# Kernel tuning notes

Hardware: AMD Instinct MI355X
Metric: run time of the kernel (lower is better)

## Reference

```python
import jax, jax.numpy as jnp
import numpy as np

H = 2048
NH = 16
DH = H // NH
EPS = 1e-05


def setup_inputs() -> dict:
    key = jax.random.key(0)
    ks = jax.random.split(key, 12)
    B, S, A = 4, 2048, 512
    s = 1.0 / np.sqrt(H)
    inp = {
        "hidden_states": jax.random.normal(ks[0], (B, S, H), jnp.float32),
        "audio_tokens": jax.random.normal(ks[1], (B, A, H), jnp.float32),
        "attention_mask": jax.random.randint(ks[2], (B, A), 0, 2).astype(jnp.float32),
        "Wq": jax.random.normal(ks[3], (H, H), jnp.float32) * s,
        "bq": jnp.zeros((H,), jnp.float32),
        "Wk": jax.random.normal(ks[4], (H, H), jnp.float32) * s,
        "bk": jnp.zeros((H,), jnp.float32),
        "Wv": jax.random.normal(ks[5], (H, H), jnp.float32) * s,
        "bv": jnp.zeros((H,), jnp.float32),
        "Wo": jax.random.normal(ks[6], (H, H), jnp.float32) * s,
        "bo": jnp.zeros((H,), jnp.float32),
        "gamma": jnp.ones((H,), jnp.float32),
        "beta": jnp.zeros((H,), jnp.float32),
    }
    return inp


def reference(hidden_states, audio_tokens, attention_mask,
              Wq, bq, Wk, bk, Wv, bv, Wo, bo, gamma, beta):
    B, S, _ = hidden_states.shape
    A = audio_tokens.shape[1]
    # projections (weights stored [in, out])
    q = (hidden_states @ Wq + bq).reshape(B, S, NH, DH)
    k = (audio_tokens @ Wk + bk).reshape(B, A, NH, DH)
    v = (audio_tokens @ Wv + bv).reshape(B, A, NH, DH)
    # scores: [B, NH, S, A]
    scores = jnp.einsum('bqhd,bkhd->bhqk', q, k) / np.sqrt(DH)
    scores = scores + attention_mask[:, None, None, :] * -10000.0
    probs = jax.nn.softmax(scores, axis=-1)
    # context: [B, S, NH, DH] -> [B, S, H]
    ctx = jnp.einsum('bhqk,bkhd->bqhd', probs, v).reshape(B, S, H)
    out = ctx @ Wo + bo
    # residual + LayerNorm
    x = out + hidden_states
    mu = jnp.mean(x, axis=-1, keepdims=True)
    var = jnp.mean(jnp.square(x - mu), axis=-1, keepdims=True)
    return (x - mu) * jax.lax.rsqrt(var + EPS) * gamma + beta
```

## Files before the change

kernel.cpp:

```cpp
#include <hip/hip_runtime.h>

#define HDIM 2048
#define NHEAD 16
#define DHEAD 128
#define BATCH 4
#define SEQ 2048
#define AUD 512

typedef unsigned short u16;
typedef unsigned int u32;
typedef __bf16 bf16_t;
typedef bf16_t bf16x8 __attribute__((ext_vector_type(8)));
typedef short short8 __attribute__((ext_vector_type(8)));
typedef float f32x4 __attribute__((ext_vector_type(4)));

typedef const __attribute__((address_space(1))) u32 gas_u32;
typedef __attribute__((address_space(3))) u32 las_u32;

__device__ __forceinline__ float b2f(u16 h) {
  union { u32 u; float f; } v; v.u = ((u32)h) << 16; return v.f;
}
__device__ __forceinline__ u16 f2b(float f) {
  union { float f; u32 u; } v; v.f = f;
  u32 r = (v.u + 0x7FFFu + ((v.u >> 16) & 1u)) >> 16;
  return (u16)r;
}

__global__ __launch_bounds__(256) void cvt2_k(const float* __restrict__ s0,
                                              u16* __restrict__ d0, int n0,
                                              const float* __restrict__ s1,
                                              u16* __restrict__ d1, int n1) {
  int i = blockIdx.x * 256 + threadIdx.x;
  const float* src; u16* dst; int j;
  if (i < n0) { src = s0; dst = d0; j = i; }
  else { j = i - n0; if (j >= n1) return; src = s1; dst = d1; }
  const float4* s4 = (const float4*)src;
  float4 a = s4[2 * j], b = s4[2 * j + 1];
  short8 o;
  o[0] = (short)f2b(a.x); o[1] = (short)f2b(a.y);
  o[2] = (short)f2b(a.z); o[3] = (short)f2b(a.w);
  o[4] = (short)f2b(b.x); o[5] = (short)f2b(b.y);
  o[6] = (short)f2b(b.z); o[7] = (short)f2b(b.w);
  *(short8*)(dst + (size_t)j * 8) = o;
}

__global__ __launch_bounds__(256) void transpose4_k(
    const float* __restrict__ Wq, const float* __restrict__ Wk,
    const float* __restrict__ Wv, const float* __restrict__ Wo,
    u16* __restrict__ dst4) {
  const float* src = (blockIdx.z == 0) ? Wq
                   : (blockIdx.z == 1) ? Wk
                   : (blockIdx.z == 2) ? Wv : Wo;
  u16* dst = dst4 + (size_t)blockIdx.z * HDIM * HDIM;
  __shared__ float tile[32][33];
  int tx = threadIdx.x, ty = threadIdx.y;
  int x = blockIdx.x * 32 + tx;
  int y0 = blockIdx.y * 32;
#pragma unroll
  for (int j = 0; j < 32; j += 8)
    tile[ty + j][tx] = src[(size_t)(y0 + ty + j) * HDIM + x];
  __syncthreads();
  int x2 = y0 + tx;
  int y2 = blockIdx.x * 32;
#pragma unroll
  for (int j = 0; j < 32; j += 8)
    dst[(size_t)(y2 + ty + j) * HDIM + x2] = f2b(tile[tx][ty + j]);
}

__global__ __launch_bounds__(256) void gemm_bt(
    const u16* __restrict__ A, int lda,
    const u16* __restrict__ Bt, int ldb,
    void* __restrict__ Cv, int ldc,
    const float* __restrict__ bias, float alpha, int M, int N, int K, int cmode) {
  __shared__ u16 As[128 * 32];
  __shared__ u16 Bs[128 * 32];

  int lane = threadIdx.x & 63;
  int wave = threadIdx.x >> 6;
  int gdx = gridDim.x;
  int id = blockIdx.y * gdx + blockIdx.x;
  int cpx = (gdx * gridDim.y) >> 3;
  int sid = (id & 7) * cpx + (id >> 3);
  int m0 = (sid / gdx) * 128;
  int n0 = (sid % gdx) * 128;
  int wm = (wave & 1) * 64;
  int wn = (wave >> 1) * 64;
  int row16 = lane & 15;
  int quad = lane >> 4;

  int sr = (lane >> 2);
  int sc = (lane & 3) * 8;

  f32x4 acc[4][4];
#pragma unroll
  for (int i = 0; i < 4; i++)
#pragma unroll
    for (int j = 0; j < 4; j++) acc[i][j] = (f32x4){0.f, 0.f, 0.f, 0.f};

  for (int k0 = 0; k0 < K; k0 += 32) {
#pragma unroll
    for (int t = 0; t < 2; t++) {
      int chunk = wave * 2 + t;
      int r = chunk * 16 + sr;
      const u16* ga = A + (size_t)(m0 + r) * lda + k0 + sc;
      const u16* gb = Bt + (size_t)(n0 + r) * ldb + k0 + sc;
      __builtin_amdgcn_global_load_lds((gas_u32*)ga, (las_u32*)(As + chunk * 512), 16, 0, 0);
      __builtin_amdgcn_global_load_lds((gas_u32*)gb, (las_u32*)(Bs + chunk * 512), 16, 0, 0);
    }
    __syncthreads();

    short8 af[4], bf[4];
#pragma unroll
    for (int mt = 0; mt < 4; mt++)
      af[mt] = *(const short8*)(As + (wm + mt * 16 + row16) * 32 + quad * 8);
#pragma unroll
    for (int nt = 0; nt < 4; nt++)
      bf[nt] = *(const short8*)(Bs + (wn + nt * 16 + row16) * 32 + quad * 8);
#pragma unroll
    for (int mt = 0; mt < 4; mt++)
#pragma unroll
      for (int nt = 0; nt < 4; nt++)
        acc[mt][nt] = __builtin_amdgcn_mfma_f32_16x16x32_bf16(
            __builtin_bit_cast(bf16x8, af[mt]), __builtin_bit_cast(bf16x8, bf[nt]),
            acc[mt][nt], 0, 0, 0);
    __syncthreads();
  }

#pragma unroll
  for (int nt = 0; nt < 4; nt++) {
    int nn = n0 + wn + nt * 16 + row16;
    float bv = bias ? bias[nn] : 0.f;
#pragma unroll
    for (int mt = 0; mt < 4; mt++) {
#pragma unroll
      for (int r = 0; r < 4; r++) {
        int mm = m0 + wm + mt * 16 + quad * 4 + r;
        float val = (acc[mt][nt][r] + bv) * alpha;
        if (cmode == 2) {
          ((float*)Cv)[(size_t)mm * ldc + nn] = val;
        } else if (cmode == 1) {
          int bb = mm >> 9, aa = mm & 511;
          int hh = nn >> 7, dd = nn & 127;
          ((u16*)Cv)[((size_t)((bb * 16 + hh) * 128 + dd)) * 512 + aa] = f2b(val);
        } else {
          ((u16*)Cv)[(size_t)mm * ldc + nn] = f2b(val);
        }
      }
    }
  }
}

__global__ __launch_bounds__(512, 2) void gemm_ring8(
    const u16* __restrict__ A, int lda,
    const u16* __restrict__ Bt, int ldb,
    void* __restrict__ Cv, int ldc,
    const float* __restrict__ bias, float alpha, int K, int cmode) {
  __shared__ u16 As[4][256 * 32];
  __shared__ u16 Bs[4][256 * 32];

  int tid = threadIdx.x;
  int lane = tid & 63, wave = tid >> 6;
  int wr = wave >> 2, wc = wave & 3;
  int row16 = lane & 15, quad = lane >> 4;
  int cofs = (quad * 8) ^ (((row16 >> 1) & 3) << 3);

  int gdx = gridDim.x;
  int id = blockIdx.y * gdx + blockIdx.x;
  int cpx = (gdx * gridDim.y) >> 3;
  int sid = (id & 7) * cpx + (id >> 3);
  int n0 = (sid % gdx) * 256;
  int m0 = (sid / gdx) * 256;

  int r0 = tid >> 2;
  int c0 = ((tid & 3) ^ ((r0 >> 1) & 3)) * 8;

  f32x4 acc[8][4];
#pragma unroll
  for (int i = 0; i < 8; i++)
#pragma unroll
    for (int j = 0; j < 4; j++) acc[i][j] = (f32x4){0.f, 0.f, 0.f, 0.f};

  auto stageA = [&](int slot, int k0) {
#pragma unroll
    for (int l = 0; l < 2; l++) {
      int row = l * 128 + r0;
      __builtin_amdgcn_global_load_lds(
          (gas_u32*)(A + (size_t)(m0 + row) * lda + k0 + c0),
          (las_u32*)(&As[slot][(l * 512 + tid) * 8]), 16, 0, 0);
    }
  };
  auto stageB = [&](int slot, int k0) {
#pragma unroll
    for (int l = 0; l < 2; l++) {
      int row = l * 128 + r0;
      __builtin_amdgcn_global_load_lds(
          (gas_u32*)(Bt + (size_t)(n0 + row) * ldb + k0 + c0),
          (las_u32*)(&Bs[slot][(l * 512 + tid) * 8]), 16, 0, 0);
    }
  };

  int NT = K >> 5;
  stageA(0, 0);  stageB(0, 0);
  stageA(1, 32); stageB(1, 32);
  stageA(2, 64); stageB(2, 64);
  asm volatile("s_waitcnt vmcnt(8)" ::: "memory");
  __builtin_amdgcn_s_barrier();

  for (int kt = 0; kt < NT; ++kt) {
    int slot = kt & 3;
    int sp = (kt + 3) & 3;
    bool pf = (kt + 3) < NT;
    const u16* as = &As[slot][0];
    const u16* bs = &Bs[slot][0];

    short8 bfr[4], af[4];
#pragma unroll
    for (int ni = 0; ni < 4; ni++)
      bfr[ni] = *(const short8*)(bs + (wc * 64 + ni * 16 + row16) * 32 + cofs);
#pragma unroll
    for (int mi = 0; mi < 4; mi++)
      af[mi] = *(const short8*)(as + (wr * 128 + mi * 16 + row16) * 32 + cofs);
    if (pf) stageA(sp, (kt + 3) << 5);
    __builtin_amdgcn_s_barrier();
    asm volatile("s_waitcnt lgkmcnt(0)" ::: "memory");
    __builtin_amdgcn_s_setprio(1);
#pragma unroll
    for (int mi = 0; mi < 4; mi++)
#pragma unroll
      for (int ni = 0; ni < 4; ni++)
        acc[mi][ni] = __builtin_amdgcn_mfma_f32_16x16x32_bf16(
            __builtin_bit_cast(bf16x8, af[mi]), __builtin_bit_cast(bf16x8, bfr[ni]),
            acc[mi][ni], 0, 0, 0);
    __builtin_amdgcn_s_setprio(0);
    __builtin_amdgcn_s_barrier();

    short8 ag[4];
#pragma unroll
    for (int mi = 0; mi < 4; mi++)
      ag[mi] = *(const short8*)(as + (wr * 128 + (mi + 4) * 16 + row16) * 32 + cofs);
    if (pf) stageB(sp, (kt + 3) << 5);
    {
      int nf = NT - 2 - kt;
      if (nf >= 2)      asm volatile("s_waitcnt vmcnt(8)" ::: "memory");
      else if (nf == 1) asm volatile("s_waitcnt vmcnt(4)" ::: "memory");
      else              asm volatile("s_waitcnt vmcnt(0)" ::: "memory");
    }
    __builtin_amdgcn_s_barrier();
    asm volatile("s_waitcnt lgkmcnt(0)" ::: "memory");
    __builtin_amdgcn_s_setprio(1);
#pragma unroll
    for (int mi = 0; mi < 4; mi++)
#pragma unroll
      for (int ni = 0; ni < 4; ni++)
        acc[mi + 4][ni] = __builtin_amdgcn_mfma_f32_16x16x32_bf16(
            __builtin_bit_cast(bf16x8, ag[mi]), __builtin_bit_cast(bf16x8, bfr[ni]),
            acc[mi + 4][ni], 0, 0, 0);
    __builtin_amdgcn_s_setprio(0);
    __builtin_amdgcn_s_barrier();
  }

#pragma unroll
  for (int ni = 0; ni < 4; ni++) {
    int nn = n0 + wc * 64 + ni * 16 + row16;
    float bv = bias ? bias[nn] : 0.f;
#pragma unroll
    for (int mi = 0; mi < 8; mi++) {
#pragma unroll
      for (int r = 0; r < 4; r++) {
        int mm = m0 + wr * 128 + mi * 16 + quad * 4 + r;
        float val = (acc[mi][ni][r] + bv) * alpha;
        if (cmode == 2) ((float*)Cv)[(size_t)mm * ldc + nn] = val;
        else            ((u16*)Cv)[(size_t)mm * ldc + nn] = f2b(val);
      }
    }
  }
}

__global__ __launch_bounds__(256) void flash_k(
    const u16* __restrict__ Q, const u16* __restrict__ K,
    const u16* __restrict__ Vt, const float* __restrict__ mask,
    u16* __restrict__ Ctx) {
  __shared__ u16 KP[128 * 128];
  __shared__ u16 Vs[128 * 128];

  int bh = blockIdx.y, b = bh >> 4, h = bh & 15;
  int q0 = blockIdx.x * 128;
  int lane = threadIdx.x & 63, wave = threadIdx.x >> 6;
  int row16 = lane & 15, quad = lane >> 4;
  int wq = wave * 32;
  int swr = (row16 & 7) << 3;

  const u16* qbase = Q + ((size_t)(b * SEQ + q0)) * HDIM + h * DHEAD;
  const u16* kbase = K + ((size_t)b * AUD) * HDIM + h * DHEAD;
  const u16* vbase = Vt + ((size_t)(b * NHEAD + h)) * DHEAD * AUD;
  const float* mp = mask + b * AUD;

  short8 qf[2][4];
#pragma unroll
  for (int mt = 0; mt < 2; mt++)
#pragma unroll
    for (int ks = 0; ks < 4; ks++)
      qf[mt][ks] = *(const short8*)(qbase + (size_t)(wq + mt * 16 + row16) * HDIM +
                                    ks * 32 + quad * 8);

  f32x4 oacc[2][8];
  float lacc[2][4];
#pragma unroll
  for (int mt = 0; mt < 2; mt++) {
#pragma unroll
    for (int nt = 0; nt < 8; nt++) oacc[mt][nt] = (f32x4){0.f, 0.f, 0.f, 0.f};
#pragma unroll
    for (int r = 0; r < 4; r++) lacc[mt][r] = 0.f;
  }

  int sl = (lane >> 4);
  int scol = (lane & 15) * 8;

#pragma unroll
  for (int t = 0; t < 8; t++) {
    int c = wave * 8 + t;
    int r = c * 4 + sl;
    int csw = scol ^ ((r & 7) << 3);
    __builtin_amdgcn_global_load_lds(
        (gas_u32*)(kbase + (size_t)r * HDIM + csw),
        (las_u32*)(KP + c * 512), 16, 0, 0);
    __builtin_amdgcn_global_load_lds(
        (gas_u32*)(vbase + (size_t)r * AUD + csw),
        (las_u32*)(Vs + c * 512), 16, 0, 0);
  }
  __syncthreads();

  for (int kt = 0; kt < 4; kt++) {
    f32x4 sacc[2][8];
#pragma unroll
    for (int mt = 0; mt < 2; mt++)
#pragma unroll
      for (int nt = 0; nt < 8; nt++) sacc[mt][nt] = (f32x4){0.f, 0.f, 0.f, 0.f};
#pragma unroll
    for (int ks = 0; ks < 4; ks++) {
      short8 bf[8];
      int cofs = (ks * 32 + quad * 8) ^ swr;
#pragma unroll
      for (int nt = 0; nt < 8; nt++)
        bf[nt] = *(const short8*)(KP + (nt * 16 + row16) * 128 + cofs);
#pragma unroll
      for (int mt = 0; mt < 2; mt++)
#pragma unroll
        for (int nt = 0; nt < 8; nt++)
          sacc[mt][nt] = __builtin_amdgcn_mfma_f32_16x16x32_bf16(
              __builtin_bit_cast(bf16x8, qf[mt][ks]), __builtin_bit_cast(bf16x8, bf[nt]),
              sacc[mt][nt], 0, 0, 0);
    }

#pragma unroll
    for (int nt = 0; nt < 8; nt++) {
      float mval = mp[kt * 128 + nt * 16 + row16] * (-10000.0f);
#pragma unroll
      for (int mt = 0; mt < 2; mt++)
#pragma unroll
        for (int r = 0; r < 4; r++) {
          float e = __expf(sacc[mt][nt][r] + mval);
          sacc[mt][nt][r] = e;
          lacc[mt][r] += e;
        }
    }

    asm volatile("s_waitcnt lgkmcnt(0)" ::: "memory");
    __builtin_amdgcn_s_barrier();

#pragma unroll
    for (int mt = 0; mt < 2; mt++)
#pragma unroll
      for (int nt = 0; nt < 8; nt++)
#pragma unroll
        for (int r = 0; r < 4; r++) {
          int prow = wq + mt * 16 + quad * 4 + r;
          KP[prow * 128 + ((nt * 16 + row16) ^ ((prow & 7) << 3))] =
              f2b(sacc[mt][nt][r]);
        }

    short8 kreg[8], vreg[8];
    if (kt < 3) {
#pragma unroll
      for (int t = 0; t < 8; t++) {
        int r = wq + t * 4 + sl;
        kreg[t] = *(const short8*)(kbase + (size_t)((kt + 1) * 128 + r) * HDIM + scol);
        vreg[t] = *(const short8*)(vbase + (size_t)r * AUD + (kt + 1) * 128 + scol);
      }
    }

#pragma unroll
    for (int ks = 0; ks < 4; ks++) {
      short8 af[2], bf[8];
      int cofs = (ks * 32 + quad * 8) ^ swr;
#pragma unroll
      for (int mt = 0; mt < 2; mt++)
        af[mt] = *(const short8*)(KP + (wq + mt * 16 + row16) * 128 + cofs);
#pragma unroll
      for (int nt = 0; nt < 8; nt++)
        bf[nt] = *(const short8*)(Vs + (nt * 16 + row16) * 128 + cofs);
#pragma unroll
      for (int mt = 0; mt < 2; mt++)
#pragma unroll
        for (int nt = 0; nt < 8; nt++)
          oacc[mt][nt] = __builtin_amdgcn_mfma_f32_16x16x32_bf16(
              __builtin_bit_cast(bf16x8, af[mt]), __builtin_bit_cast(bf16x8, bf[nt]),
              oacc[mt][nt], 0, 0, 0);
    }

    asm volatile("s_waitcnt lgkmcnt(0)" ::: "memory");
    __builtin_amdgcn_s_barrier();

    if (kt < 3) {
      asm volatile("s_waitcnt vmcnt(0)" ::: "memory");
#pragma unroll
      for (int t = 0; t < 8; t++) {
        int r = wq + t * 4 + sl;
        int cs = scol ^ ((r & 7) << 3);
        *(short8*)(KP + r * 128 + cs) = kreg[t];
        *(short8*)(Vs + r * 128 + cs) = vreg[t];
      }
    }
    asm volatile("s_waitcnt lgkmcnt(0)" ::: "memory");
    __builtin_amdgcn_s_barrier();
  }

#pragma unroll
  for (int mt = 0; mt < 2; mt++)
#pragma unroll
    for (int r = 0; r < 4; r++) {
      float s = lacc[mt][r];
      for (int off = 1; off < 16; off <<= 1) s += __shfl_xor(s, off, 64);
      lacc[mt][r] = 1.0f / s;
    }

  u16* cb = Ctx + ((size_t)(b * SEQ + q0 + wq)) * HDIM + h * DHEAD;
#pragma unroll
  for (int mt = 0; mt < 2; mt++)
#pragma unroll
    for (int nt = 0; nt < 8; nt++)
#pragma unroll
      for (int r = 0; r < 4; r++)
        cb[(size_t)(mt * 16 + quad * 4 + r) * HDIM + nt * 16 + row16] =
            f2b(oacc[mt][nt][r] * lacc[mt][r]);
}

__global__ __launch_bounds__(256) void ln_k(const float* O,
                                            const float* __restrict__ hs,
                                            const float* __restrict__ gamma,
                                            const float* __restrict__ beta,
                                            float* out) {
  size_t rowoff = (size_t)blockIdx.x * HDIM;
  float x[8], sum = 0.f, sq = 0.f;
#pragma unroll
  for (int i = 0; i < 8; i++) {
    int idx = threadIdx.x + 256 * i;
    float v = O[rowoff + idx] + hs[rowoff + idx];
    x[i] = v;
    sum += v;
    sq += v * v;
  }
  for (int off = 32; off; off >>= 1) {
    sum += __shfl_xor(sum, off, 64);
    sq += __shfl_xor(sq, off, 64);
  }
  __shared__ float red[8];
  int wave = threadIdx.x >> 6, lane = threadIdx.x & 63;
  if (lane == 0) { red[wave] = sum; red[4 + wave] = sq; }
  __syncthreads();
  sum = red[0] + red[1] + red[2] + red[3];
  sq = red[4] + red[5] + red[6] + red[7];
  float mu = sum * (1.0f / HDIM);
  float var = sq * (1.0f / HDIM) - mu * mu;
  float inv = rsqrtf(var + 1e-5f);
#pragma unroll
  for (int i = 0; i < 8; i++) {
    int idx = threadIdx.x + 256 * i;
    out[rowoff + idx] = (x[i] - mu) * inv * gamma[idx] + beta[idx];
  }
}

extern "C" void kernel_launch(void* const* d_in, const int* in_sizes, int n_in,
                              void* d_out, int out_size, void* d_ws, size_t ws_size,
                              hipStream_t stream) {
  (void)in_sizes; (void)n_in; (void)out_size; (void)ws_size;
  const float* hs   = (const float*)d_in[0];
  const float* at   = (const float*)d_in[1];
  const float* mask = (const float*)d_in[2];
  const float* Wq = (const float*)d_in[3];  const float* bq = (const float*)d_in[4];
  const float* Wk = (const float*)d_in[5];  const float* bk = (const float*)d_in[6];
  const float* Wv = (const float*)d_in[7];  const float* bv = (const float*)d_in[8];
  const float* Wo = (const float*)d_in[9];  const float* bo = (const float*)d_in[10];
  const float* gamma = (const float*)d_in[11];
  const float* beta  = (const float*)d_in[12];
  float* out = (float*)d_out;
  u16* ws = (u16*)d_ws;

  u16* hsb = ws;
  u16* atb = ws + 16777216;
  u16* wT4 = ws + 20971520;
  u16* Q   = ws + 37748736;
  u16* Kb  = ws + 54525952;
  u16* Vt  = ws + 58720256;
  u16* Ctx = ws + 62914560;
  u16* wTq = wT4;
  u16* wTk = wT4 + 4194304;
  u16* wTv = wT4 + 8388608;
  u16* wTo = wT4 + 12582912;

  cvt2_k<<<10240, 256, 0, stream>>>(hs, hsb, 2097152, at, atb, 524288);
  transpose4_k<<<dim3(64, 64, 4), dim3(32, 8), 0, stream>>>(Wq, Wk, Wv, Wo, wT4);

  const float qscale = 0.08838834764831845f;

  gemm_ring8<<<dim3(8, 32), 512, 0, stream>>>(hsb, HDIM, wTq, HDIM, Q, HDIM,
                                              bq, qscale, 2048, 0);
  gemm_bt<<<dim3(16, 16), 256, 0, stream>>>(atb, HDIM, wTk, HDIM, Kb, HDIM,
                                            bk, 1.0f, 2048, 2048, 2048, 0);
  gemm_bt<<<dim3(16, 16), 256, 0, stream>>>(atb, HDIM, wTv, HDIM, Vt, HDIM,
                                            bv, 1.0f, 2048, 2048, 2048, 1);

  flash_k<<<dim3(SEQ / 128, BATCH * NHEAD), 256, 0, stream>>>(Q, Kb, Vt, mask, Ctx);

  gemm_ring8<<<dim3(8, 32), 512, 0, stream>>>(Ctx, HDIM, wTo, HDIM, out, HDIM,
                                              bo, 1.0f, 2048, 2);
  ln_k<<<8192, 256, 0, stream>>>(out, hs, gamma, beta, out);
}
```

Measured before the change: 594.0 us.

## Use 8 waves per flash attention block and swizzle block order

The attention kernel now launches 512 threads per block, with each wave owning 16 query rows instead of 32. This halves the per-thread accumulator and Q-fragment registers, and the launch bound asks for 4 blocks per CU to raise occupancy. Block IDs are also remapped so consecutive blocks spread across batch-head groups, likely to balance work or cache locality across XCDs. In exchange, each K/V B-fragment read from LDS now feeds half as many MFMAs, so LDS traffic per FLOP doubles.

Result: slower. 740.8 us (+24.7%).

```diff
diff --git a/kernel.cpp b/kernel.cpp
--- a/kernel.cpp
+++ b/kernel.cpp
@@ -276,18 +276,22 @@
   }
 }
 
-__global__ __launch_bounds__(256) void flash_k(
+__global__ __launch_bounds__(512, 4) void flash_k(
     const u16* __restrict__ Q, const u16* __restrict__ K,
     const u16* __restrict__ Vt, const float* __restrict__ mask,
     u16* __restrict__ Ctx) {
   __shared__ u16 KP[128 * 128];
   __shared__ u16 Vs[128 * 128];
 
-  int bh = blockIdx.y, b = bh >> 4, h = bh & 15;
-  int q0 = blockIdx.x * 128;
+  int id = blockIdx.y * gridDim.x + blockIdx.x;
+  int sid = (id & 7) * 128 + (id >> 3);
+  int qt = sid & 15, bh = sid >> 4;
+  int b = bh >> 4, h = bh & 15;
+  int q0 = qt * 128;
+
   int lane = threadIdx.x & 63, wave = threadIdx.x >> 6;
   int row16 = lane & 15, quad = lane >> 4;
-  int wq = wave * 32;
+  int wq = wave * 16;
   int swr = (row16 & 7) << 3;
 
   const u16* qbase = Q + ((size_t)(b * SEQ + q0)) * HDIM + h * DHEAD;
@@ -295,30 +299,24 @@
   const u16* vbase = Vt + ((size_t)(b * NHEAD + h)) * DHEAD * AUD;
   const float* mp = mask + b * AUD;
 
-  short8 qf[2][4];
-#pragma unroll
-  for (int mt = 0; mt < 2; mt++)
-#pragma unroll
-    for (int ks = 0; ks < 4; ks++)
-      qf[mt][ks] = *(const short8*)(qbase + (size_t)(wq + mt * 16 + row16) * HDIM +
-                                    ks * 32 + quad * 8);
-
-  f32x4 oacc[2][8];
-  float lacc[2][4];
-#pragma unroll
-  for (int mt = 0; mt < 2; mt++) {
-#pragma unroll
-    for (int nt = 0; nt < 8; nt++) oacc[mt][nt] = (f32x4){0.f, 0.f, 0.f, 0.f};
-#pragma unroll
-    for (int r = 0; r < 4; r++) lacc[mt][r] = 0.f;
-  }
+  short8 qf[4];
+#pragma unroll
+  for (int ks = 0; ks < 4; ks++)
+    qf[ks] = *(const short8*)(qbase + (size_t)(wq + row16) * HDIM + ks * 32 + quad * 8);
+
+  f32x4 oacc[8];
+  float lacc[4];
+#pragma unroll
+  for (int nt = 0; nt < 8; nt++) oacc[nt] = (f32x4){0.f, 0.f, 0.f, 0.f};
+#pragma unroll
+  for (int r = 0; r < 4; r++) lacc[r] = 0.f;
 
   int sl = (lane >> 4);
   int scol = (lane & 15) * 8;
 
 #pragma unroll
-  for (int t = 0; t < 8; t++) {
-    int c = wave * 8 + t;
+  for (int t = 0; t < 4; t++) {
+    int c = wave * 4 + t;
     int r = c * 4 + sl;
     int csw = scol ^ ((r & 7) << 3);
     __builtin_amdgcn_global_load_lds(
@@ -331,11 +329,9 @@
   __syncthreads();
 
   for (int kt = 0; kt < 4; kt++) {
-    f32x4 sacc[2][8];
-#pragma unroll
-    for (int mt = 0; mt < 2; mt++)
-#pragma unroll
-      for (int nt = 0; nt < 8; nt++) sacc[mt][nt] = (f32x4){0.f, 0.f, 0.f, 0.f};
+    f32x4 sacc[8];
+#pragma unroll
+    for (int nt = 0; nt < 8; nt++) sacc[nt] = (f32x4){0.f, 0.f, 0.f, 0.f};
 #pragma unroll
     for (int ks = 0; ks < 4; ks++) {
       short8 bf[8];
@@ -344,45 +340,38 @@
       for (int nt = 0; nt < 8; nt++)
         bf[nt] = *(const short8*)(KP + (nt * 16 + row16) * 128 + cofs);
 #pragma unroll
-      for (int mt = 0; mt < 2; mt++)
-#pragma unroll
-        for (int nt = 0; nt < 8; nt++)
-          sacc[mt][nt] = __builtin_amdgcn_mfma_f32_16x16x32_bf16(
-              __builtin_bit_cast(bf16x8, qf[mt][ks]), __builtin_bit_cast(bf16x8, bf[nt]),
-              sacc[mt][nt], 0, 0, 0);
+      for (int nt = 0; nt < 8; nt++)
+        sacc[nt] = __builtin_amdgcn_mfma_f32_16x16x32_bf16(
+            __builtin_bit_cast(bf16x8, qf[ks]), __builtin_bit_cast(bf16x8, bf[nt]),
+            sacc[nt], 0, 0, 0);
     }
 
 #pragma unroll
     for (int nt = 0; nt < 8; nt++) {
       float mval = mp[kt * 128 + nt * 16 + row16] * (-10000.0f);
 #pragma unroll
-      for (int mt = 0; mt < 2; mt++)
-#pragma unroll
-        for (int r = 0; r < 4; r++) {
-          float e = __expf(sacc[mt][nt][r] + mval);
-          sacc[mt][nt][r] = e;
-          lacc[mt][r] += e;
-        }
+      for (int r = 0; r < 4; r++) {
+        float e = __expf(sacc[nt][r] + mval);
+        sacc[nt][r] = e;
+        lacc[r] += e;
+      }
     }
 
     asm volatile("s_waitcnt lgkmcnt(0)" ::: "memory");
     __builtin_amdgcn_s_barrier();
 
 #pragma unroll
-    for (int mt = 0; mt < 2; mt++)
-#pragma unroll
-      for (int nt = 0; nt < 8; nt++)
-#pragma unroll
-        for (int r = 0; r < 4; r++) {
-          int prow = wq + mt * 16 + quad * 4 + r;
-          KP[prow * 128 + ((nt * 16 + row16) ^ ((prow & 7) << 3))] =
-              f2b(sacc[mt][nt][r]);
-        }
-
-    short8 kreg[8], vreg[8];
+    for (int nt = 0; nt < 8; nt++)
+#pragma unroll
+      for (int r = 0; r < 4; r++) {
+        int prow = wq + quad * 4 + r;
+        KP[prow * 128 + ((nt * 16 + row16) ^ ((prow & 7) << 3))] = f2b(sacc[nt][r]);
+      }
+
+    short8 kreg[4], vreg[4];
     if (kt < 3) {
 #pragma unroll
-      for (int t = 0; t < 8; t++) {
+      for (int t = 0; t < 4; t++) {
         int r = wq + t * 4 + sl;
         kreg[t] = *(const short8*)(kbase + (size_t)((kt + 1) * 128 + r) * HDIM + scol);
         vreg[t] = *(const short8*)(vbase + (size_t)r * AUD + (kt + 1) * 128 + scol);
@@ -391,21 +380,17 @@
 
 #pragma unroll
     for (int ks = 0; ks < 4; ks++) {
-      short8 af[2], bf[8];
+      short8 af, bf[8];
       int cofs = (ks * 32 + quad * 8) ^ swr;
-#pragma unroll
-      for (int mt = 0; mt < 2; mt++)
-        af[mt] = *(const short8*)(KP + (wq + mt * 16 + row16) * 128 + cofs);
+      af = *(const short8*)(KP + (wq + row16) * 128 + cofs);
 #pragma unroll
       for (int nt = 0; nt < 8; nt++)
         bf[nt] = *(const short8*)(Vs + (nt * 16 + row16) * 128 + cofs);
 #pragma unroll
-      for (int mt = 0; mt < 2; mt++)
-#pragma unroll
-        for (int nt = 0; nt < 8; nt++)
-          oacc[mt][nt] = __builtin_amdgcn_mfma_f32_16x16x32_bf16(
-              __builtin_bit_cast(bf16x8, af[mt]), __builtin_bit_cast(bf16x8, bf[nt]),
-              oacc[mt][nt], 0, 0, 0);
+      for (int nt = 0; nt < 8; nt++)
+        oacc[nt] = __builtin_amdgcn_mfma_f32_16x16x32_bf16(
+            __builtin_bit_cast(bf16x8, af), __builtin_bit_cast(bf16x8, bf[nt]),
+            oacc[nt], 0, 0, 0);
     }
 
     asm volatile("s_waitcnt lgkmcnt(0)" ::: "memory");
@@ -414,7 +399,7 @@
     if (kt < 3) {
       asm volatile("s_waitcnt vmcnt(0)" ::: "memory");
 #pragma unroll
-      for (int t = 0; t < 8; t++) {
+      for (int t = 0; t < 4; t++) {
         int r = wq + t * 4 + sl;
         int cs = scol ^ ((r & 7) << 3);
         *(short8*)(KP + r * 128 + cs) = kreg[t];
@@ -426,23 +411,19 @@
   }
 
 #pragma unroll
-  for (int mt = 0; mt < 2; mt++)
-#pragma unroll
-    for (int r = 0; r < 4; r++) {
-      float s = lacc[mt][r];
-      for (int off = 1; off < 16; off <<= 1) s += __shfl_xor(s, off, 64);
-      lacc[mt][r] = 1.0f / s;
-    }
+  for (int r = 0; r < 4; r++) {
+    float s = lacc[r];
+    for (int off = 1; off < 16; off <<= 1) s += __shfl_xor(s, off, 64);
+    lacc[r] = 1.0f / s;
+  }
 
   u16* cb = Ctx + ((size_t)(b * SEQ + q0 + wq)) * HDIM + h * DHEAD;
 #pragma unroll
-  for (int mt = 0; mt < 2; mt++)
-#pragma unroll
-    for (int nt = 0; nt < 8; nt++)
-#pragma unroll
-      for (int r = 0; r < 4; r++)
-        cb[(size_t)(mt * 16 + quad * 4 + r) * HDIM + nt * 16 + row16] =
-            f2b(oacc[mt][nt][r] * lacc[mt][r]);
+  for (int nt = 0; nt < 8; nt++)
+#pragma unroll
+    for (int r = 0; r < 4; r++)
+      cb[(size_t)(quad * 4 + r) * HDIM + nt * 16 + row16] =
+          f2b(oacc[nt][r] * lacc[r]);
 }
 
 __global__ __launch_bounds__(256) void ln_k(const float* O,
@@ -520,7 +501,7 @@
   gemm_bt<<<dim3(16, 16), 256, 0, stream>>>(atb, HDIM, wTv, HDIM, Vt, HDIM,
                                             bv, 1.0f, 2048, 2048, 2048, 1);
 
-  flash_k<<<dim3(SEQ / 128, BATCH * NHEAD), 256, 0, stream>>>(Q, Kb, Vt, mask, Ctx);
+  flash_k<<<dim3(SEQ / 128, BATCH * NHEAD), 512, 0, stream>>>(Q, Kb, Vt, mask, Ctx);
 
   gemm_ring8<<<dim3(8, 32), 512, 0, stream>>>(Ctx, HDIM, wTo, HDIM, out, HDIM,
                                               bo, 1.0f, 2048, 2);
```
